# Kernel tuning notes

Hardware: AMD Instinct MI355X
Metric: run time of the kernel (lower is better)

## Reference

```python
import jax, jax.numpy as jnp
import numpy as np

B = 16384       # batch of peptide samples
M = 15          # max_peptide_size
R = 64          # aa_rep_size
P = 34          # number of pocket positions
F = 9           # filter_size
A = 20          # alphabet size


def setup_inputs() -> dict:
    key = jax.random.key(0)
    k1, k2, k3, k4 = jax.random.split(key, 4)
    peptide_encoding = jax.random.normal(k1, (B, M, R), dtype=jnp.float32)
    pocket_aa_idx = jax.random.randint(k2, (B, P), 0, A, dtype=jnp.int32)
    adj_mask = jax.random.randint(k3, (B, P, M), 0, 2, dtype=jnp.int32)
    # one trainable 1-D filter of length F per alphabet letter ('uniform' init)
    kernels = jax.random.uniform(k4, (A, F), dtype=jnp.float32, minval=-0.05, maxval=0.05)
    return {"peptide_encoding": peptide_encoding, "pocket_aa_idx": pocket_aa_idx,
            "adj_mask": adj_mask, "kernels": kernels}


def reference(peptide_encoding, pocket_aa_idx, adj_mask, kernels):
    # Per pocket position p of sample b: filter = kernels[pocket_aa_idx[b,p]]  [B,P,F]
    filt = kernels[pocket_aa_idx]
    # Convolution is linear, so sum the adjacent peptide-position encodings first:
    # s[b,p,r] = sum_m adj_mask[b,p,m] * peptide_encoding[b,m,r]   -> [B,P,R]
    s = jnp.einsum('bpm,bmr->bpr', adj_mask.astype(peptide_encoding.dtype), peptide_encoding)
    # Full convolution along the representation axis: output length R + F - 1
    conv1 = jax.vmap(jax.vmap(lambda a, b: jnp.convolve(a, b, mode='full')))
    out = conv1(s, filt)  # [B, P, R+F-1]
    return out
```

## Files before the change

kernel.cpp:

```cpp
#include <hip/hip_runtime.h>

#define MM 15
#define RR 64
#define PP 34
#define FF 9
#define AA 20
#define OW 72
#define SP 84
#define KS 12
#define AJ 17
#define AJROWS 48

__global__ __launch_bounds__(256)
void ppc_kernel(const float* __restrict__ pe,
                const int*   __restrict__ idx,
                const int*   __restrict__ adj,
                const float* __restrict__ kernels,
                float*       __restrict__ out)
{
    const int b = blockIdx.x;
    const int t = threadIdx.x;

    __shared__ float s_pe[MM * RR];
    __shared__ float s_kern[AA * KS];
    __shared__ float s_adjf[AJROWS * AJ];
    __shared__ int   s_idx[PP];
    __shared__ float s_s[PP * SP];

    const float* peb  = pe  + (size_t)b * (MM * RR);
    const int*   adjb = adj + (size_t)b * (PP * MM);

    if (t < (MM * RR) / 4)
        *(float4*)&s_pe[t * 4] = *(const float4*)&peb[t * 4];
    for (int i = t; i < AA * FF; i += 256) {
        int a = (unsigned)i / FF, j = i - a * FF;
        s_kern[a * KS + j] = kernels[i];
    }
    for (int i = t; i < PP * MM; i += 256) {
        int p = (unsigned)i / MM, m = i - p * MM;
        s_adjf[p * AJ + m] = (float)adjb[i];
    }
    if (t < (AJROWS - PP) * AJ) s_adjf[PP * AJ + t] = 0.0f;
    if (t < PP) s_idx[t] = idx[(size_t)b * PP + t];
    for (int i = t; i < PP * 20; i += 256) {
        int p = (unsigned)i / 20, c = i - p * 20;
        s_s[p * SP + (c < 8 ? c : 64 + c)] = 0.0f;
    }
    __syncthreads();

    {
        const int c  = t & 15;
        const int q  = t >> 4;
        const int r0 = c << 2;
        const float* g0 = &s_adjf[(q)      * AJ];
        const float* g1 = &s_adjf[(q + 16) * AJ];
        const float* g2 = &s_adjf[(q + 32) * AJ];
        float ax0=0,ay0=0,az0=0,aw0=0;
        float ax1=0,ay1=0,az1=0,aw1=0;
        float ax2=0,ay2=0,az2=0,aw2=0;
        #pragma unroll
        for (int m = 0; m < MM; ++m) {
            const float4 v = *(const float4*)&s_pe[m * RR + r0];
            const float ga = g0[m], gb = g1[m], gc = g2[m];
            ax0 += ga * v.x; ay0 += ga * v.y; az0 += ga * v.z; aw0 += ga * v.w;
            ax1 += gb * v.x; ay1 += gb * v.y; az1 += gb * v.z; aw1 += gb * v.w;
            ax2 += gc * v.x; ay2 += gc * v.y; az2 += gc * v.z; aw2 += gc * v.w;
        }
        *(float4*)&s_s[(q)      * SP + 8 + r0] = make_float4(ax0, ay0, az0, aw0);
        *(float4*)&s_s[(q + 16) * SP + 8 + r0] = make_float4(ax1, ay1, az1, aw1);
        if (q + 32 < PP)
            *(float4*)&s_s[(q + 32) * SP + 8 + r0] = make_float4(ax2, ay2, az2, aw2);
    }
    __syncthreads();

    float* outb = out + (size_t)b * (PP * OW);
    for (int i = t; i < PP * 18; i += 256) {
        const int p  = (unsigned)i / 18u;
        const int o0 = (i - p * 18) << 2;

        float w[12];
        {
            const float* base = &s_s[p * SP + o0];
            *(float4*)&w[0] = *(const float4*)&base[0];
            *(float4*)&w[4] = *(const float4*)&base[4];
            *(float4*)&w[8] = *(const float4*)&base[8];
        }
        float kf[KS];
        {
            const float* kb = &s_kern[s_idx[p] * KS];
            *(float4*)&kf[0] = *(const float4*)&kb[0];
            *(float4*)&kf[4] = *(const float4*)&kb[4];
            kf[8] = kb[8];
        }
        float ax = 0.f, ay = 0.f, az = 0.f, aw = 0.f;
        #pragma unroll
        for (int j = 0; j < FF; ++j) {
            const float k = kf[j];
            ax += k * w[8  - j];
            ay += k * w[9  - j];
            az += k * w[10 - j];
            aw += k * w[11 - j];
        }
        *(float4*)&outb[p * OW + o0] = make_float4(ax, ay, az, aw);
    }
}

extern "C" void kernel_launch(void* const* d_in, const int* in_sizes, int n_in,
                              void* d_out, int out_size, void* d_ws, size_t ws_size,
                              hipStream_t stream) {
    const float* pe      = (const float*)d_in[0];
    const int*   idx     = (const int*)  d_in[1];
    const int*   adj     = (const int*)  d_in[2];
    const float* kernels = (const float*)d_in[3];
    float*       out     = (float*)d_out;

    const int B = in_sizes[0] / (MM * RR);
    ppc_kernel<<<B, 256, 0, stream>>>(pe, idx, adj, kernels, out);
}
```

Baseline: 78.00 us.

## Keep adjacency sums in registers and build conv windows via wave shuffles

After: 134.2 us. 72.1% more time.

```diff
diff --git a/kernel.cpp b/kernel.cpp
--- a/kernel.cpp
+++ b/kernel.cpp
@@ -6,9 +6,8 @@
 #define FF 9
 #define AA 20
 #define OW 72
-#define SP 84
 #define KS 12
-#define AJ 17
+#define AJ 20
 #define AJROWS 48
 
 __global__ __launch_bounds__(256)
@@ -25,74 +24,83 @@
     __shared__ float s_kern[AA * KS];
     __shared__ float s_adjf[AJROWS * AJ];
     __shared__ int   s_idx[PP];
-    __shared__ float s_s[PP * SP];
 
     const float* peb  = pe  + (size_t)b * (MM * RR);
     const int*   adjb = adj + (size_t)b * (PP * MM);
 
+    for (int i = t; i < AJROWS * AJ; i += 256) s_adjf[i] = 0.0f;
     if (t < (MM * RR) / 4)
         *(float4*)&s_pe[t * 4] = *(const float4*)&peb[t * 4];
-    for (int i = t; i < AA * FF; i += 256) {
-        int a = (unsigned)i / FF, j = i - a * FF;
-        s_kern[a * KS + j] = kernels[i];
+    if (t < AA * FF) {
+        int a = (unsigned)t / FF, j = t - a * FF;
+        s_kern[a * KS + j] = kernels[t];
     }
+    if (t < PP) s_idx[t] = idx[(size_t)b * PP + t];
+    __syncthreads();
     for (int i = t; i < PP * MM; i += 256) {
         int p = (unsigned)i / MM, m = i - p * MM;
         s_adjf[p * AJ + m] = (float)adjb[i];
     }
-    if (t < (AJROWS - PP) * AJ) s_adjf[PP * AJ + t] = 0.0f;
-    if (t < PP) s_idx[t] = idx[(size_t)b * PP + t];
-    for (int i = t; i < PP * 20; i += 256) {
-        int p = (unsigned)i / 20, c = i - p * 20;
-        s_s[p * SP + (c < 8 ? c : 64 + c)] = 0.0f;
-    }
     __syncthreads();
 
+    const int c  = t & 15;
+    const int q  = t >> 4;
+    const int r0 = c << 2;
+
+    float4 S0, S1, S2;
     {
-        const int c  = t & 15;
-        const int q  = t >> 4;
-        const int r0 = c << 2;
         const float* g0 = &s_adjf[(q)      * AJ];
         const float* g1 = &s_adjf[(q + 16) * AJ];
         const float* g2 = &s_adjf[(q + 32) * AJ];
-        float ax0=0,ay0=0,az0=0,aw0=0;
-        float ax1=0,ay1=0,az1=0,aw1=0;
-        float ax2=0,ay2=0,az2=0,aw2=0;
+        float x0=0,y0=0,z0=0,w0=0, x1=0,y1=0,z1=0,w1=0, x2=0,y2=0,z2=0,w2=0;
         #pragma unroll
-        for (int m = 0; m < MM; ++m) {
-            const float4 v = *(const float4*)&s_pe[m * RR + r0];
-            const float ga = g0[m], gb = g1[m], gc = g2[m];
-            ax0 += ga * v.x; ay0 += ga * v.y; az0 += ga * v.z; aw0 += ga * v.w;
-            ax1 += gb * v.x; ay1 += gb * v.y; az1 += gb * v.z; aw1 += gb * v.w;
-            ax2 += gc * v.x; ay2 += gc * v.y; az2 += gc * v.z; aw2 += gc * v.w;
+        for (int mc = 0; mc < 4; ++mc) {
+            const float4 a0 = *(const float4*)&g0[mc * 4];
+            const float4 a1 = *(const float4*)&g1[mc * 4];
+            const float4 a2 = *(const float4*)&g2[mc * 4];
+            #pragma unroll
+            for (int mm = 0; mm < 4; ++mm) {
+                const int m = mc * 4 + mm;
+                if (m < MM) {
+                    const float4 v = *(const float4*)&s_pe[m * RR + r0];
+                    const float ga = (&a0.x)[mm], gb = (&a1.x)[mm], gc = (&a2.x)[mm];
+                    x0 += ga*v.x; y0 += ga*v.y; z0 += ga*v.z; w0 += ga*v.w;
+                    x1 += gb*v.x; y1 += gb*v.y; z1 += gb*v.z; w1 += gb*v.w;
+                    x2 += gc*v.x; y2 += gc*v.y; z2 += gc*v.z; w2 += gc*v.w;
+                }
+            }
         }
-        *(float4*)&s_s[(q)      * SP + 8 + r0] = make_float4(ax0, ay0, az0, aw0);
-        *(float4*)&s_s[(q + 16) * SP + 8 + r0] = make_float4(ax1, ay1, az1, aw1);
-        if (q + 32 < PP)
-            *(float4*)&s_s[(q + 32) * SP + 8 + r0] = make_float4(ax2, ay2, az2, aw2);
+        S0 = make_float4(x0,y0,z0,w0);
+        S1 = make_float4(x1,y1,z1,w1);
+        S2 = make_float4(x2,y2,z2,w2);
     }
-    __syncthreads();
 
     float* outb = out + (size_t)b * (PP * OW);
-    for (int i = t; i < PP * 18; i += 256) {
-        const int p  = (unsigned)i / 18u;
-        const int o0 = (i - p * 18) << 2;
+
+    auto conv_p = [&](const float4 S, const int p) {
+        float kf[FF];
+        {
+            const int a = (p < PP) ? s_idx[p] : 0;
+            const float* kb = &s_kern[a * KS];
+            const float4 k0 = *(const float4*)&kb[0];
+            const float4 k1 = *(const float4*)&kb[4];
+            kf[0]=k0.x; kf[1]=k0.y; kf[2]=k0.z; kf[3]=k0.w;
+            kf[4]=k1.x; kf[5]=k1.y; kf[6]=k1.z; kf[7]=k1.w;
+            kf[8]=kb[8];
+        }
+        float4 SM1, SM2, SP1;
+        SM1.x=__shfl_up(S.x,1); SM1.y=__shfl_up(S.y,1); SM1.z=__shfl_up(S.z,1); SM1.w=__shfl_up(S.w,1);
+        SM2.x=__shfl_up(S.x,2); SM2.y=__shfl_up(S.y,2); SM2.z=__shfl_up(S.z,2); SM2.w=__shfl_up(S.w,2);
+        SP1.x=__shfl_down(S.x,1); SP1.y=__shfl_down(S.y,1); SP1.z=__shfl_down(S.z,1); SP1.w=__shfl_down(S.w,1);
+        if (c < 1) SM1 = make_float4(0,0,0,0);
+        if (c < 2) SM2 = make_float4(0,0,0,0);
 
         float w[12];
-        {
-            const float* base = &s_s[p * SP + o0];
-            *(float4*)&w[0] = *(const float4*)&base[0];
-            *(float4*)&w[4] = *(const float4*)&base[4];
-            *(float4*)&w[8] = *(const float4*)&base[8];
-        }
-        float kf[KS];
-        {
-            const float* kb = &s_kern[s_idx[p] * KS];
-            *(float4*)&kf[0] = *(const float4*)&kb[0];
-            *(float4*)&kf[4] = *(const float4*)&kb[4];
-            kf[8] = kb[8];
-        }
-        float ax = 0.f, ay = 0.f, az = 0.f, aw = 0.f;
+        w[0]=SM2.x; w[1]=SM2.y; w[2] =SM2.z; w[3] =SM2.w;
+        w[4]=SM1.x; w[5]=SM1.y; w[6] =SM1.z; w[7] =SM1.w;
+        w[8]=S.x;   w[9]=S.y;   w[10]=S.z;   w[11]=S.w;
+
+        float ax=0, ay=0, az=0, aw=0;
         #pragma unroll
         for (int j = 0; j < FF; ++j) {
             const float k = kf[j];
@@ -101,8 +109,32 @@
             az += k * w[10 - j];
             aw += k * w[11 - j];
         }
-        *(float4*)&outb[p * OW + o0] = make_float4(ax, ay, az, aw);
-    }
+        if (p < PP)
+            *(float4*)&outb[p * OW + r0] = make_float4(ax, ay, az, aw);
+
+        if (c >= 14 && p < PP) {
+            float wt[12];
+            wt[0]=S.x; wt[1]=S.y; wt[2]=S.z; wt[3]=S.w;
+            if (c == 14) { wt[4]=SP1.x; wt[5]=SP1.y; wt[6]=SP1.z; wt[7]=SP1.w; }
+            else         { wt[4]=0;     wt[5]=0;     wt[6]=0;     wt[7]=0;     }
+            wt[8]=0; wt[9]=0; wt[10]=0; wt[11]=0;
+            float tx=0, ty=0, tz=0, tw=0;
+            #pragma unroll
+            for (int j = 0; j < FF; ++j) {
+                const float k = kf[j];
+                tx += k * wt[8  - j];
+                ty += k * wt[9  - j];
+                tz += k * wt[10 - j];
+                tw += k * wt[11 - j];
+            }
+            const int o0 = (c == 14) ? 64 : 68;
+            *(float4*)&outb[p * OW + o0] = make_float4(tx, ty, tz, tw);
+        }
+    };
+
+    conv_p(S0, q);
+    conv_p(S1, q + 16);
+    conv_p(S2, q + 32);
 }
 
 extern "C" void kernel_launch(void* const* d_in, const int* in_sizes, int n_in,
```
